# Optimization experiments

Hardware: AMD Instinct MI355X
Metric: run time of the kernel (lower is better)

Reference implementation:

```python
import jax, jax.numpy as jnp
import numpy as np

H = 512          # hidden_size == input_size
K = 32768        # number of child cell inputs (lattice merge fan-in)


def setup_inputs() -> dict:
    key = jax.random.key(0)
    ks = jax.random.split(key, 8)
    s = 1.0 / np.sqrt(H)  # keep matmul outputs O(1)
    return {
        "input_": jax.random.normal(ks[0], (1, H), dtype=jnp.float32),
        "c_input": jax.random.normal(ks[1], (K, H), dtype=jnp.float32),
        "h_0": jax.random.normal(ks[2], (1, H), dtype=jnp.float32),
        "c_0": jax.random.normal(ks[3], (1, H), dtype=jnp.float32),
        "weight_ih": jax.random.normal(ks[4], (H, 3 * H), dtype=jnp.float32) * s,
        "weight_hh": jax.random.normal(ks[5], (H, 3 * H), dtype=jnp.float32) * s,
        "bias": jnp.zeros((3 * H,), dtype=jnp.float32),
        "alpha_weight_ih": jax.random.normal(ks[6], (H, H), dtype=jnp.float32) * s,
        "alpha_weight_hh": jax.random.normal(ks[7], (H, H), dtype=jnp.float32) * s,
    }


def reference(input_, c_input, h_0, c_0, weight_ih, weight_hh, bias,
              alpha_weight_ih, alpha_weight_hh):
    # Gate pre-activations: addmm(bias, h_0, W_hh) + input_ @ W_ih  -> [1, 3H]
    gates = h_0 @ weight_hh + bias + input_ @ weight_ih
    i, o, g = jnp.split(gates, 3, axis=1)        # each [1, H]
    i = jax.nn.sigmoid(i)
    o = jax.nn.sigmoid(o)
    g = jnp.tanh(g)

    # Variable-child softmax-weighted cell merge (non-empty c_input branch)
    alpha_wi = input_ @ alpha_weight_ih          # [1, H], broadcast over K
    alpha_wh = c_input @ alpha_weight_hh         # [K, H]
    alpha = jax.nn.sigmoid(alpha_wi + alpha_wh)  # [K, H]

    logits = jnp.concatenate([i, alpha], axis=0)  # [K+1, H]
    w = jnp.exp(logits)
    w = w / (w.sum(axis=0, keepdims=True) + 1e-12)

    merge = jnp.concatenate([g, c_input], axis=0)  # [K+1, H]
    c_1 = (merge * w).sum(axis=0, keepdims=True)   # [1, H]
    h_1 = o * jnp.tanh(c_1)                        # [1, H]
    return h_1, c_1
```

## Files before the change

### kernel.cpp

```cpp
#include <hip/hip_runtime.h>
#include <hip/hip_bf16.h>
#include <stdint.h>

#define Hdim 512
#define KC   32768

typedef __hip_bfloat16 bf16;
typedef __attribute__((ext_vector_type(8))) short short8;
typedef __attribute__((ext_vector_type(4))) float float4v;

__device__ __forceinline__ unsigned int pack_bf16_trunc(float e0, float e1) {
  union { float f; unsigned int u; } a, b;
  a.f = e0; b.f = e1;
  return __builtin_amdgcn_perm(b.u, a.u, 0x07060302u);
}

__device__ __forceinline__ unsigned long long pack64(float4v v) {
  return (unsigned long long)pack_bf16_trunc(v[0], v[1])
       | ((unsigned long long)pack_bf16_trunc(v[2], v[3]) << 32);
}

__global__ __launch_bounds__(256) void prep_wt_kernel(
    const float* __restrict__ input_, const float* __restrict__ h_0,
    const float* __restrict__ w_ih, const float* __restrict__ w_hh,
    const float* __restrict__ a_w_ih, const float* __restrict__ a_w_hh,
    float* __restrict__ gates, float* __restrict__ awi, bf16* __restrict__ wt) {
  __shared__ float sh[64 * 65];
  const int t = threadIdx.x;
  const int b = blockIdx.x;
  if (b < 32) {
    const int lane = t & 63, wv = t >> 6;
    float* h0s = sh;
    float* ins = sh + 512;
    float* red = sh + 1024;
    for (int i = t; i < 512; i += 256) { h0s[i] = h_0[i]; ins[i] = input_[i]; }
    __syncthreads();
    float acc = 0.f;
    if (b < 24) {
      const int j = b * 64 + lane;
      const float* whh = w_hh + j;
      const float* wih = w_ih + j;
#pragma unroll 16
      for (int i = 0; i < 128; ++i) {
        const int d = wv * 128 + i;
        acc += h0s[d] * whh[(size_t)d * 1536] + ins[d] * wih[(size_t)d * 1536];
      }
    } else {
      const int j = (b - 24) * 64 + lane;
      const float* wai = a_w_ih + j;
#pragma unroll 16
      for (int i = 0; i < 128; ++i) {
        const int d = wv * 128 + i;
        acc += ins[d] * wai[(size_t)d * Hdim];
      }
    }
    red[wv * 64 + lane] = acc;
    __syncthreads();
    if (t < 64) {
      float s = red[t] + red[64 + t] + red[128 + t] + red[192 + t];
      if (b < 24) gates[b * 64 + t] = s;
      else        awi[(b - 24) * 64 + t] = s;
    }
  } else {
    const int bb = b - 32;
    const int d0 = (bb & 7) * 64, h0 = (bb >> 3) * 64;
    const int tx = t & 63, tw = t >> 6;
    float (*tile)[65] = (float (*)[65])sh;
#pragma unroll
    for (int r = 0; r < 16; ++r) {
      const int row = r * 4 + tw;
      tile[row][tx] = a_w_hh[(size_t)(d0 + row) * Hdim + h0 + tx];
    }
    __syncthreads();
#pragma unroll
    for (int r = 0; r < 16; ++r) {
      const int row = r * 4 + tw;
      wt[(size_t)(h0 + row) * Hdim + d0 + tx] = __float2bfloat16(tile[tx][row]);
    }
  }
}

__global__ __launch_bounds__(256, 3) void gemm_reduce_kernel(
    const float* __restrict__ c_input, const bf16* __restrict__ WT,
    const float* __restrict__ awi,
    float* __restrict__ pw, float* __restrict__ pwc) {
  __shared__ __align__(16) bf16 As[128 * 64];
  __shared__ __align__(16) bf16 Bs[128 * 64];
  __shared__ float red_w[2][128];
  __shared__ float red_wc[2][128];

  const int tid  = threadIdx.x;
  const int lane = tid & 63;
  const int wave = tid >> 6;
  const int wm   = wave & 1;
  const int wn   = wave >> 1;
  const int lm   = lane & 15;
  const int lq   = lane >> 4;

  const int id     = blockIdx.x;
  const int kk_idx = ((id >> 5) << 3) | (id & 7);
  const int h_idx  = (id >> 3) & 3;
  const int kk0 = kk_idx * 128;
  const int h0  = h_idx * 128;

  char* AsB = (char*)As;
  char* BsB = (char*)Bs;

  const int sub   = tid & 15;
  const int rbase = tid >> 4;
  const float* aglob = c_input + (size_t)(kk0 + rbase) * Hdim + sub * 4;
  const int a_lds = rbase * 128 + (((sub >> 1) ^ (rbase & 7)) * 16) + (sub & 1) * 8;

  const int brow0 = wave * 8 + (lane >> 3);
  const int bg    = lane & 7;
  const bf16* bglob = WT + (size_t)(h0 + brow0) * Hdim + bg * 8;
  const int b_lds = brow0 * 128 + ((bg ^ (lane >> 3)) * 16);

  float4v acc[4][4];
#pragma unroll
  for (int i = 0; i < 4; ++i)
#pragma unroll
    for (int j = 0; j < 4; ++j)
      acc[i][j] = (float4v){0.f, 0.f, 0.f, 0.f};

  float4v ap[8];
  short8  bp[4];

#pragma unroll
  for (int j = 0; j < 8; ++j)
    ap[j] = *(const float4v*)(aglob + j * 16 * Hdim);
#pragma unroll
  for (int r = 0; r < 4; ++r)
    bp[r] = *(const short8*)(bglob + (size_t)r * 32 * Hdim);
#pragma unroll
  for (int j = 0; j < 8; ++j)
    *(unsigned long long*)(AsB + j * 2048 + a_lds) = pack64(ap[j]);
#pragma unroll
  for (int r = 0; r < 4; ++r)
    *(short8*)(BsB + r * 4096 + b_lds) = bp[r];
  __syncthreads();

  for (int t = 0; t < 8; ++t) {
    const int d0n = (t + 1) * 64;
    if (t < 7) {
#pragma unroll
      for (int j = 0; j < 8; ++j)
        ap[j] = *(const float4v*)(aglob + j * 16 * Hdim + d0n);
#pragma unroll
      for (int r = 0; r < 4; ++r)
        bp[r] = *(const short8*)(bglob + (size_t)r * 32 * Hdim + d0n);
    }
#pragma unroll
    for (int ks = 0; ks < 2; ++ks) {
      short8 a[4], bfr[4];
#pragma unroll
      for (int mt = 0; mt < 4; ++mt) {
        const int row = wm * 64 + mt * 16 + lm;
        a[mt] = *(const short8*)(AsB + row * 128 + (((ks * 4 + lq) ^ (lm & 7)) * 16));
      }
#pragma unroll
      for (int nt = 0; nt < 4; ++nt) {
        const int row = wn * 64 + nt * 16 + lm;
        bfr[nt] = *(const short8*)(BsB + row * 128 + (((ks * 4 + lq) ^ (lm & 7)) * 16));
      }
#pragma unroll
      for (int mt = 0; mt < 4; ++mt)
#pragma unroll
        for (int nt = 0; nt < 4; ++nt)
          acc[mt][nt] = __builtin_amdgcn_mfma_f32_16x16x32_bf16(a[mt], bfr[nt], acc[mt][nt], 0, 0, 0);
    }
    __syncthreads();
    if (t < 7) {
#pragma unroll
      for (int j = 0; j < 8; ++j)
        *(unsigned long long*)(AsB + j * 2048 + a_lds) = pack64(ap[j]);
#pragma unroll
      for (int r = 0; r < 4; ++r)
        *(short8*)(BsB + r * 4096 + b_lds) = bp[r];
    }
    __syncthreads();
  }

  float awi_l[4];
#pragma unroll
  for (int nt = 0; nt < 4; ++nt)
    awi_l[nt] = awi[h0 + wn * 64 + nt * 16 + lm];

  float sw[4] = {0.f, 0.f, 0.f, 0.f}, swc[4] = {0.f, 0.f, 0.f, 0.f};
#pragma unroll
  for (int nt = 0; nt < 4; ++nt) {
    const int h = h0 + wn * 64 + nt * 16 + lm;
#pragma unroll
    for (int mt = 0; mt < 4; ++mt) {
      const int kkb = kk0 + wm * 64 + mt * 16 + lq * 4;
#pragma unroll
      for (int r = 0; r < 4; ++r) {
        float v = acc[mt][nt][r] + awi_l[nt];
        float aval = 1.f / (1.f + __expf(-v));
        float e = __expf(aval);
        float c = c_input[(size_t)(kkb + r) * Hdim + h];
        sw[nt]  += e;
        swc[nt] += e * c;
      }
    }
  }
#pragma unroll
  for (int nt = 0; nt < 4; ++nt) {
    sw[nt]  += __shfl_xor(sw[nt], 16, 64);
    sw[nt]  += __shfl_xor(sw[nt], 32, 64);
    swc[nt] += __shfl_xor(swc[nt], 16, 64);
    swc[nt] += __shfl_xor(swc[nt], 32, 64);
  }
  if (lq == 0) {
#pragma unroll
    for (int nt = 0; nt < 4; ++nt) {
      red_w[wm][wn * 64 + nt * 16 + lm]  = sw[nt];
      red_wc[wm][wn * 64 + nt * 16 + lm] = swc[nt];
    }
  }
  __syncthreads();
  if (tid < 128) {
    pw[(size_t)kk_idx * Hdim + h0 + tid]  = red_w[0][tid] + red_w[1][tid];
    pwc[(size_t)kk_idx * Hdim + h0 + tid] = red_wc[0][tid] + red_wc[1][tid];
  }
}

__global__ __launch_bounds__(256) void finalize_kernel(
    const float* __restrict__ pw, const float* __restrict__ pwc,
    const float* __restrict__ gates, const float* __restrict__ bias,
    float* __restrict__ out) {
  __shared__ float rsw[8][32], rswc[8][32];
  const int t = threadIdx.x;
  const int hl = t & 31, q = t >> 5;
  const int hh = blockIdx.x * 32 + hl;
  float sw = 0.f, swc = 0.f;
#pragma unroll 8
  for (int kb = q * 32; kb < q * 32 + 32; ++kb) {
    sw  += pw[(size_t)kb * Hdim + hh];
    swc += pwc[(size_t)kb * Hdim + hh];
  }
  rsw[q][hl] = sw; rswc[q][hl] = swc;
  __syncthreads();
  if (t < 32) {
    const int h = blockIdx.x * 32 + t;
    sw = 0.f; swc = 0.f;
#pragma unroll
    for (int q2 = 0; q2 < 8; ++q2) { sw += rsw[q2][t]; swc += rswc[q2][t]; }
    float ipre = gates[h] + bias[h];
    float opre = gates[Hdim + h] + bias[Hdim + h];
    float gpre = gates[2 * Hdim + h] + bias[2 * Hdim + h];
    float ei = expf(1.f / (1.f + expf(-ipre)));
    float g  = tanhf(gpre);
    float o  = 1.f / (1.f + expf(-opre));
    float denom = ei + sw + 1e-12f;
    float c1 = (ei * g + swc) / denom;
    float h1 = o * tanhf(c1);
    out[h]        = h1;
    out[Hdim + h] = c1;
  }
}

extern "C" void kernel_launch(void* const* d_in, const int* in_sizes, int n_in,
                              void* d_out, int out_size, void* d_ws, size_t ws_size,
                              hipStream_t stream) {
  const float* input_  = (const float*)d_in[0];
  const float* c_input = (const float*)d_in[1];
  const float* h_0     = (const float*)d_in[2];
  const float* w_ih    = (const float*)d_in[4];
  const float* w_hh    = (const float*)d_in[5];
  const float* bias    = (const float*)d_in[6];
  const float* a_w_ih  = (const float*)d_in[7];
  const float* a_w_hh  = (const float*)d_in[8];

  char* ws = (char*)d_ws;
  float* pw    = (float*)ws;
  float* pwc   = (float*)(ws + 512 * 1024);
  float* gates = (float*)(ws + 1024 * 1024);
  float* awi   = (float*)(ws + 1024 * 1024 + 6144);
  bf16*  WT    = (bf16*)(ws + 1024 * 1024 + 8192);

  hipLaunchKernelGGL(prep_wt_kernel, dim3(96), dim3(256), 0, stream,
                     input_, h_0, w_ih, w_hh, a_w_ih, a_w_hh, gates, awi, WT);
  hipLaunchKernelGGL(gemm_reduce_kernel, dim3(1024), dim3(256), 0, stream,
                     c_input, WT, awi, pw, pwc);
  hipLaunchKernelGGL(finalize_kernel, dim3(16), dim3(256), 0, stream,
                     pw, pwc, gates, bias, (float*)d_out);
}
```

Baseline: 153.3 us.

## Load GEMM fragments directly from global memory into registers, bypassing LDS

```diff
diff --git a/kernel.cpp b/kernel.cpp
--- a/kernel.cpp
+++ b/kernel.cpp
@@ -13,11 +13,6 @@
   union { float f; unsigned int u; } a, b;
   a.f = e0; b.f = e1;
   return __builtin_amdgcn_perm(b.u, a.u, 0x07060302u);
-}
-
-__device__ __forceinline__ unsigned long long pack64(float4v v) {
-  return (unsigned long long)pack_bf16_trunc(v[0], v[1])
-       | ((unsigned long long)pack_bf16_trunc(v[2], v[3]) << 32);
 }
 
 __global__ __launch_bounds__(256) void prep_wt_kernel(
@@ -80,12 +75,10 @@
   }
 }
 
-__global__ __launch_bounds__(256, 3) void gemm_reduce_kernel(
+__global__ __launch_bounds__(256, 2) void gemm_reduce_kernel(
     const float* __restrict__ c_input, const bf16* __restrict__ WT,
     const float* __restrict__ awi,
     float* __restrict__ pw, float* __restrict__ pwc) {
-  __shared__ __align__(16) bf16 As[128 * 64];
-  __shared__ __align__(16) bf16 Bs[128 * 64];
   __shared__ float red_w[2][128];
   __shared__ float red_wc[2][128];
 
@@ -103,18 +96,14 @@
   const int kk0 = kk_idx * 128;
   const int h0  = h_idx * 128;
 
-  char* AsB = (char*)As;
-  char* BsB = (char*)Bs;
-
-  const int sub   = tid & 15;
-  const int rbase = tid >> 4;
-  const float* aglob = c_input + (size_t)(kk0 + rbase) * Hdim + sub * 4;
-  const int a_lds = rbase * 128 + (((sub >> 1) ^ (rbase & 7)) * 16) + (sub & 1) * 8;
-
-  const int brow0 = wave * 8 + (lane >> 3);
-  const int bg    = lane & 7;
-  const bf16* bglob = WT + (size_t)(h0 + brow0) * Hdim + bg * 8;
-  const int b_lds = brow0 * 128 + ((bg ^ (lane >> 3)) * 16);
+  const float* aptr[4];
+  const bf16*  bptr[4];
+#pragma unroll
+  for (int mt = 0; mt < 4; ++mt)
+    aptr[mt] = c_input + (size_t)(kk0 + wm * 64 + mt * 16 + lm) * Hdim + lq * 8;
+#pragma unroll
+  for (int nt = 0; nt < 4; ++nt)
+    bptr[nt] = WT + (size_t)(h0 + wn * 64 + nt * 16 + lm) * Hdim + lq * 8;
 
   float4v acc[4][4];
 #pragma unroll
@@ -123,63 +112,51 @@
     for (int j = 0; j < 4; ++j)
       acc[i][j] = (float4v){0.f, 0.f, 0.f, 0.f};
 
-  float4v ap[8];
-  short8  bp[4];
-
-#pragma unroll
-  for (int j = 0; j < 8; ++j)
-    ap[j] = *(const float4v*)(aglob + j * 16 * Hdim);
-#pragma unroll
-  for (int r = 0; r < 4; ++r)
-    bp[r] = *(const short8*)(bglob + (size_t)r * 32 * Hdim);
-#pragma unroll
-  for (int j = 0; j < 8; ++j)
-    *(unsigned long long*)(AsB + j * 2048 + a_lds) = pack64(ap[j]);
-#pragma unroll
-  for (int r = 0; r < 4; ++r)
-    *(short8*)(BsB + r * 4096 + b_lds) = bp[r];
-  __syncthreads();
-
-  for (int t = 0; t < 8; ++t) {
-    const int d0n = (t + 1) * 64;
-    if (t < 7) {
-#pragma unroll
-      for (int j = 0; j < 8; ++j)
-        ap[j] = *(const float4v*)(aglob + j * 16 * Hdim + d0n);
-#pragma unroll
-      for (int r = 0; r < 4; ++r)
-        bp[r] = *(const short8*)(bglob + (size_t)r * 32 * Hdim + d0n);
-    }
-#pragma unroll
-    for (int ks = 0; ks < 2; ++ks) {
-      short8 a[4], bfr[4];
-#pragma unroll
-      for (int mt = 0; mt < 4; ++mt) {
-        const int row = wm * 64 + mt * 16 + lm;
-        a[mt] = *(const short8*)(AsB + row * 128 + (((ks * 4 + lq) ^ (lm & 7)) * 16));
-      }
-#pragma unroll
-      for (int nt = 0; nt < 4; ++nt) {
-        const int row = wn * 64 + nt * 16 + lm;
-        bfr[nt] = *(const short8*)(BsB + row * 128 + (((ks * 4 + lq) ^ (lm & 7)) * 16));
-      }
-#pragma unroll
-      for (int mt = 0; mt < 4; ++mt)
-#pragma unroll
-        for (int nt = 0; nt < 4; ++nt)
-          acc[mt][nt] = __builtin_amdgcn_mfma_f32_16x16x32_bf16(a[mt], bfr[nt], acc[mt][nt], 0, 0, 0);
-    }
-    __syncthreads();
-    if (t < 7) {
-#pragma unroll
-      for (int j = 0; j < 8; ++j)
-        *(unsigned long long*)(AsB + j * 2048 + a_lds) = pack64(ap[j]);
-#pragma unroll
-      for (int r = 0; r < 4; ++r)
-        *(short8*)(BsB + r * 4096 + b_lds) = bp[r];
-    }
-    __syncthreads();
-  }
+  float4v A0[8], A1[8];
+  short8  B0[4], B1[4];
+
+#define LOAD_STEP(S, AR, BR)                                          \
+  do {                                                                \
+    _Pragma("unroll")                                                 \
+    for (int mt = 0; mt < 4; ++mt) {                                  \
+      AR[mt * 2]     = *(const float4v*)(aptr[mt] + (S) * 32);        \
+      AR[mt * 2 + 1] = *(const float4v*)(aptr[mt] + (S) * 32 + 4);    \
+    }                                                                 \
+    _Pragma("unroll")                                                 \
+    for (int nt = 0; nt < 4; ++nt)                                    \
+      BR[nt] = *(const short8*)(bptr[nt] + (S) * 32);                 \
+  } while (0)
+
+#define COMPUTE_STEP(AR, BR)                                          \
+  do {                                                                \
+    short8 af[4];                                                     \
+    _Pragma("unroll")                                                 \
+    for (int mt = 0; mt < 4; ++mt) {                                  \
+      union { unsigned int w[4]; short8 s8; } u;                      \
+      u.w[0] = pack_bf16_trunc(AR[mt * 2][0], AR[mt * 2][1]);         \
+      u.w[1] = pack_bf16_trunc(AR[mt * 2][2], AR[mt * 2][3]);         \
+      u.w[2] = pack_bf16_trunc(AR[mt * 2 + 1][0], AR[mt * 2 + 1][1]); \
+      u.w[3] = pack_bf16_trunc(AR[mt * 2 + 1][2], AR[mt * 2 + 1][3]); \
+      af[mt] = u.s8;                                                  \
+    }                                                                 \
+    _Pragma("unroll")                                                 \
+    for (int mt = 0; mt < 4; ++mt)                                    \
+      _Pragma("unroll")                                               \
+      for (int nt = 0; nt < 4; ++nt)                                  \
+        acc[mt][nt] = __builtin_amdgcn_mfma_f32_16x16x32_bf16(        \
+            af[mt], BR[nt], acc[mt][nt], 0, 0, 0);                    \
+  } while (0)
+
+  LOAD_STEP(0, A0, B0);
+#pragma unroll
+  for (int s = 0; s < 16; s += 2) {
+    LOAD_STEP(s + 1, A1, B1);
+    COMPUTE_STEP(A0, B0);
+    if (s + 2 < 16) LOAD_STEP(s + 2, A0, B0);
+    COMPUTE_STEP(A1, B1);
+  }
+#undef LOAD_STEP
+#undef COMPUTE_STEP
 
   float awi_l[4];
 #pragma unroll
```

After: 222.4 us. +45.1%, slower.

## Double-buffer LDS tiles in gemm_reduce to drop one barrier per k-step

Applied to the files above, without the earlier changes.

```diff
diff --git a/kernel.cpp b/kernel.cpp
--- a/kernel.cpp
+++ b/kernel.cpp
@@ -80,12 +80,12 @@
   }
 }
 
-__global__ __launch_bounds__(256, 3) void gemm_reduce_kernel(
+__global__ __launch_bounds__(256) void gemm_reduce_kernel(
     const float* __restrict__ c_input, const bf16* __restrict__ WT,
     const float* __restrict__ awi,
     float* __restrict__ pw, float* __restrict__ pwc) {
-  __shared__ __align__(16) bf16 As[128 * 64];
-  __shared__ __align__(16) bf16 Bs[128 * 64];
+  __shared__ __align__(16) bf16 AsBuf[2][128 * 64];
+  __shared__ __align__(16) bf16 BsBuf[2][128 * 64];
   __shared__ float red_w[2][128];
   __shared__ float red_wc[2][128];
 
@@ -103,17 +103,19 @@
   const int kk0 = kk_idx * 128;
   const int h0  = h_idx * 128;
 
-  char* AsB = (char*)As;
-  char* BsB = (char*)Bs;
+  char* const As0 = (char*)AsBuf[0];
+  char* const As1 = (char*)AsBuf[1];
+  char* const Bs0 = (char*)BsBuf[0];
+  char* const Bs1 = (char*)BsBuf[1];
 
   const int sub   = tid & 15;
   const int rbase = tid >> 4;
-  const float* aglob = c_input + (size_t)(kk0 + rbase) * Hdim + sub * 4;
+  const float* aglobS = c_input + (size_t)(kk0 + rbase) * Hdim + sub * 4;
   const int a_lds = rbase * 128 + (((sub >> 1) ^ (rbase & 7)) * 16) + (sub & 1) * 8;
 
   const int brow0 = wave * 8 + (lane >> 3);
   const int bg    = lane & 7;
-  const bf16* bglob = WT + (size_t)(h0 + brow0) * Hdim + bg * 8;
+  const bf16* bglobS = WT + (size_t)(h0 + brow0) * Hdim + bg * 8;
   const int b_lds = brow0 * 128 + ((bg ^ (lane >> 3)) * 16);
 
   float4v acc[4][4];
@@ -123,63 +125,78 @@
     for (int j = 0; j < 4; ++j)
       acc[i][j] = (float4v){0.f, 0.f, 0.f, 0.f};
 
-  float4v ap[8];
-  short8  bp[4];
-
-#pragma unroll
-  for (int j = 0; j < 8; ++j)
-    ap[j] = *(const float4v*)(aglob + j * 16 * Hdim);
-#pragma unroll
-  for (int r = 0; r < 4; ++r)
-    bp[r] = *(const short8*)(bglob + (size_t)r * 32 * Hdim);
-#pragma unroll
-  for (int j = 0; j < 8; ++j)
-    *(unsigned long long*)(AsB + j * 2048 + a_lds) = pack64(ap[j]);
-#pragma unroll
-  for (int r = 0; r < 4; ++r)
-    *(short8*)(BsB + r * 4096 + b_lds) = bp[r];
+  {
+    float4v ap[8]; short8 bp[4];
+#pragma unroll
+    for (int j = 0; j < 8; ++j)
+      ap[j] = *(const float4v*)(aglobS + j * 16 * Hdim);
+#pragma unroll
+    for (int r = 0; r < 4; ++r)
+      bp[r] = *(const short8*)(bglobS + (size_t)r * 32 * Hdim);
+#pragma unroll
+    for (int j = 0; j < 8; ++j)
+      *(unsigned long long*)(As0 + j * 2048 + a_lds) = pack64(ap[j]);
+#pragma unroll
+    for (int r = 0; r < 4; ++r)
+      *(short8*)(Bs0 + r * 4096 + b_lds) = bp[r];
+  }
   __syncthreads();
 
-  for (int t = 0; t < 8; ++t) {
-    const int d0n = (t + 1) * 64;
-    if (t < 7) {
-#pragma unroll
-      for (int j = 0; j < 8; ++j)
-        ap[j] = *(const float4v*)(aglob + j * 16 * Hdim + d0n);
-#pragma unroll
-      for (int r = 0; r < 4; ++r)
-        bp[r] = *(const short8*)(bglob + (size_t)r * 32 * Hdim + d0n);
-    }
-#pragma unroll
-    for (int ks = 0; ks < 2; ++ks) {
-      short8 a[4], bfr[4];
-#pragma unroll
-      for (int mt = 0; mt < 4; ++mt) {
-        const int row = wm * 64 + mt * 16 + lm;
-        a[mt] = *(const short8*)(AsB + row * 128 + (((ks * 4 + lq) ^ (lm & 7)) * 16));
-      }
-#pragma unroll
-      for (int nt = 0; nt < 4; ++nt) {
-        const int row = wn * 64 + nt * 16 + lm;
-        bfr[nt] = *(const short8*)(BsB + row * 128 + (((ks * 4 + lq) ^ (lm & 7)) * 16));
-      }
-#pragma unroll
-      for (int mt = 0; mt < 4; ++mt)
-#pragma unroll
-        for (int nt = 0; nt < 4; ++nt)
-          acc[mt][nt] = __builtin_amdgcn_mfma_f32_16x16x32_bf16(a[mt], bfr[nt], acc[mt][nt], 0, 0, 0);
-    }
-    __syncthreads();
-    if (t < 7) {
-#pragma unroll
-      for (int j = 0; j < 8; ++j)
-        *(unsigned long long*)(AsB + j * 2048 + a_lds) = pack64(ap[j]);
-#pragma unroll
-      for (int r = 0; r < 4; ++r)
-        *(short8*)(BsB + r * 4096 + b_lds) = bp[r];
-    }
-    __syncthreads();
-  }
+#define GITER(T, RAs, RBs, WAs, WBs, NOT_LAST)                              \
+  do {                                                                      \
+    float4v ap[8]; short8 bp[4];                                            \
+    if (NOT_LAST) {                                                         \
+      const int dn = ((T) + 1) * 64;                                        \
+      _Pragma("unroll")                                                     \
+      for (int j = 0; j < 8; ++j)                                           \
+        ap[j] = *(const float4v*)(aglobS + j * 16 * Hdim + dn);             \
+      _Pragma("unroll")                                                     \
+      for (int r = 0; r < 4; ++r)                                           \
+        bp[r] = *(const short8*)(bglobS + (size_t)r * 32 * Hdim + dn);      \
+    }                                                                       \
+    __builtin_amdgcn_sched_barrier(0);   \
+    _Pragma("unroll")                                                       \
+    for (int ks = 0; ks < 2; ++ks) {                                        \
+      short8 a[4], bfr[4];                                                  \
+      _Pragma("unroll")                                                     \
+      for (int mt = 0; mt < 4; ++mt) {                                      \
+        const int row = wm * 64 + mt * 16 + lm;                             \
+        a[mt] = *(const short8*)(RAs + row * 128 +                          \
+                                 (((ks * 4 + lq) ^ (lm & 7)) * 16));        \
+      }                                                                     \
+      _Pragma("unroll")                                                     \
+      for (int nt = 0; nt < 4; ++nt) {                                      \
+        const int row = wn * 64 + nt * 16 + lm;                             \
+        bfr[nt] = *(const short8*)(RBs + row * 128 +                        \
+                                   (((ks * 4 + lq) ^ (lm & 7)) * 16));      \
+      }                                                                     \
+      _Pragma("unroll")                                                     \
+      for (int mt = 0; mt < 4; ++mt)                                        \
+        _Pragma("unroll")                                                   \
+        for (int nt = 0; nt < 4; ++nt)                                      \
+          acc[mt][nt] = __builtin_amdgcn_mfma_f32_16x16x32_bf16(            \
+              a[mt], bfr[nt], acc[mt][nt], 0, 0, 0);                        \
+    }                                                                       \
+    if (NOT_LAST) {                                                         \
+      _Pragma("unroll")                                                     \
+      for (int j = 0; j < 8; ++j)                                           \
+        *(unsigned long long*)(WAs + j * 2048 + a_lds) = pack64(ap[j]);     \
+      _Pragma("unroll")                                                     \
+      for (int r = 0; r < 4; ++r)                                           \
+        *(short8*)(WBs + r * 4096 + b_lds) = bp[r];                         \
+    }                                                                       \
+    __syncthreads();                                                        \
+  } while (0)
+
+  GITER(0, As0, Bs0, As1, Bs1, 1);
+  GITER(1, As1, Bs1, As0, Bs0, 1);
+  GITER(2, As0, Bs0, As1, Bs1, 1);
+  GITER(3, As1, Bs1, As0, Bs0, 1);
+  GITER(4, As0, Bs0, As1, Bs1, 1);
+  GITER(5, As1, Bs1, As0, Bs0, 1);
+  GITER(6, As0, Bs0, As1, Bs1, 1);
+  GITER(7, As1, Bs1, As0, Bs0, 0);
+#undef GITER
 
   float awi_l[4];
 #pragma unroll
```

After: 147.3 us. 3.9% less time.

## Widen GEMM tile to full hidden dim and stream weights via direct LDS loads

Applied to the files above, without the earlier changes.

```diff
diff --git a/kernel.cpp b/kernel.cpp
--- a/kernel.cpp
+++ b/kernel.cpp
@@ -8,6 +8,9 @@
 typedef __hip_bfloat16 bf16;
 typedef __attribute__((ext_vector_type(8))) short short8;
 typedef __attribute__((ext_vector_type(4))) float float4v;
+
+typedef const __attribute__((address_space(1))) void gvoid;
+typedef __attribute__((address_space(3))) void svoid;
 
 __device__ __forceinline__ unsigned int pack_bf16_trunc(float e0, float e1) {
   union { float f; unsigned int u; } a, b;
@@ -18,6 +21,10 @@
 __device__ __forceinline__ unsigned long long pack64(float4v v) {
   return (unsigned long long)pack_bf16_trunc(v[0], v[1])
        | ((unsigned long long)pack_bf16_trunc(v[2], v[3]) << 32);
+}
+
+__device__ __forceinline__ void gload_lds16(const void* g, void* l) {
+  __builtin_amdgcn_global_load_lds((gvoid*)g, (svoid*)l, 16, 0, 0);
 }
 
 __global__ __launch_bounds__(256) void prep_wt_kernel(
@@ -80,14 +87,16 @@
   }
 }
 
-__global__ __launch_bounds__(256, 3) void gemm_reduce_kernel(
+__global__ __launch_bounds__(512, 2) void gemm_reduce_kernel(
     const float* __restrict__ c_input, const bf16* __restrict__ WT,
     const float* __restrict__ awi,
     float* __restrict__ pw, float* __restrict__ pwc) {
-  __shared__ __align__(16) bf16 As[128 * 64];
-  __shared__ __align__(16) bf16 Bs[128 * 64];
-  __shared__ float red_w[2][128];
-  __shared__ float red_wc[2][128];
+  __shared__ __align__(16) char pool[147456];
+  char* const AsB = pool;
+  char* const Bs0 = pool + 16384;
+  char* const Bs1 = pool + 16384 + 65536;
+  float* const red_w  = (float*)pool;
+  float* const red_wc = (float*)(pool + 4096);
 
   const int tid  = threadIdx.x;
   const int lane = tid & 63;
@@ -97,99 +106,93 @@
   const int lm   = lane & 15;
   const int lq   = lane >> 4;
 
-  const int id     = blockIdx.x;
-  const int kk_idx = ((id >> 5) << 3) | (id & 7);
-  const int h_idx  = (id >> 3) & 3;
+  const int kk_idx = blockIdx.x;
   const int kk0 = kk_idx * 128;
-  const int h0  = h_idx * 128;
-
-  char* AsB = (char*)As;
-  char* BsB = (char*)Bs;
 
   const int sub   = tid & 15;
   const int rbase = tid >> 4;
-  const float* aglob = c_input + (size_t)(kk0 + rbase) * Hdim + sub * 4;
+  const float* aglobS = c_input + (size_t)(kk0 + rbase) * Hdim + sub * 4;
   const int a_lds = rbase * 128 + (((sub >> 1) ^ (rbase & 7)) * 16) + (sub & 1) * 8;
 
-  const int brow0 = wave * 8 + (lane >> 3);
-  const int bg    = lane & 7;
-  const bf16* bglob = WT + (size_t)(h0 + brow0) * Hdim + bg * 8;
-  const int b_lds = brow0 * 128 + ((bg ^ (lane >> 3)) * 16);
-
-  float4v acc[4][4];
+  const bf16* bsrcS = WT + (size_t)(64 * wave + (lane >> 3)) * Hdim
+                         + ((lane & 7) ^ (lane >> 3)) * 8;
+  const int b_lds_wave = wave * 8192;
+
+  float4v acc[4][8];
 #pragma unroll
   for (int i = 0; i < 4; ++i)
 #pragma unroll
+    for (int j = 0; j < 8; ++j)
+      acc[i][j] = (float4v){0.f, 0.f, 0.f, 0.f};
+
+#pragma unroll
+  for (int j = 0; j < 8; ++j)
+    gload_lds16(bsrcS + j * 8 * Hdim, Bs0 + b_lds_wave + j * 1024);
+  {
+    float4v ap[4];
+#pragma unroll
     for (int j = 0; j < 4; ++j)
-      acc[i][j] = (float4v){0.f, 0.f, 0.f, 0.f};
-
-  float4v ap[8];
-  short8  bp[4];
-
-#pragma unroll
-  for (int j = 0; j < 8; ++j)
-    ap[j] = *(const float4v*)(aglob + j * 16 * Hdim);
-#pragma unroll
-  for (int r = 0; r < 4; ++r)
-    bp[r] = *(const short8*)(bglob + (size_t)r * 32 * Hdim);
-#pragma unroll
-  for (int j = 0; j < 8; ++j)
-    *(unsigned long long*)(AsB + j * 2048 + a_lds) = pack64(ap[j]);
-#pragma unroll
-  for (int r = 0; r < 4; ++r)
-    *(short8*)(BsB + r * 4096 + b_lds) = bp[r];
+      ap[j] = *(const float4v*)(aglobS + (size_t)j * 32 * Hdim);
+#pragma unroll
+    for (int j = 0; j < 4; ++j)
+      *(unsigned long long*)(AsB + j * 4096 + a_lds) = pack64(ap[j]);
+  }
   __syncthreads();
 
   for (int t = 0; t < 8; ++t) {
-    const int d0n = (t + 1) * 64;
+    char* const BsR = (t & 1) ? Bs1 : Bs0;
+    char* const BsW = (t & 1) ? Bs0 : Bs1;
+    float4v ap[4];
     if (t < 7) {
+      const int dn = (t + 1) * 64;
 #pragma unroll
       for (int j = 0; j < 8; ++j)
-        ap[j] = *(const float4v*)(aglob + j * 16 * Hdim + d0n);
-#pragma unroll
-      for (int r = 0; r < 4; ++r)
-        bp[r] = *(const short8*)(bglob + (size_t)r * 32 * Hdim + d0n);
-    }
+        gload_lds16(bsrcS + j * 8 * Hdim + dn, BsW + b_lds_wave + j * 1024);
+#pragma unroll
+      for (int j = 0; j < 4; ++j)
+        ap[j] = *(const float4v*)(aglobS + (size_t)j * 32 * Hdim + dn);
+    }
+    __builtin_amdgcn_sched_barrier(0);
 #pragma unroll
     for (int ks = 0; ks < 2; ++ks) {
-      short8 a[4], bfr[4];
+      short8 a[4], bfr[8];
 #pragma unroll
       for (int mt = 0; mt < 4; ++mt) {
         const int row = wm * 64 + mt * 16 + lm;
         a[mt] = *(const short8*)(AsB + row * 128 + (((ks * 4 + lq) ^ (lm & 7)) * 16));
       }
 #pragma unroll
-      for (int nt = 0; nt < 4; ++nt) {
-        const int row = wn * 64 + nt * 16 + lm;
-        bfr[nt] = *(const short8*)(BsB + row * 128 + (((ks * 4 + lq) ^ (lm & 7)) * 16));
+      for (int nt = 0; nt < 8; ++nt) {
+        const int row = wn * 128 + nt * 16 + lm;
+        bfr[nt] = *(const short8*)(BsR + row * 128 + (((ks * 4 + lq) ^ (lm & 7)) * 16));
       }
 #pragma unroll
       for (int mt = 0; mt < 4; ++mt)
 #pragma unroll
-        for (int nt = 0; nt < 4; ++nt)
-          acc[mt][nt] = __builtin_amdgcn_mfma_f32_16x16x32_bf16(a[mt], bfr[nt], acc[mt][nt], 0, 0, 0);
+        for (int nt = 0; nt < 8; ++nt)
+          acc[mt][nt] = __builtin_amdgcn_mfma_f32_16x16x32_bf16(
+              a[mt], bfr[nt], acc[mt][nt], 0, 0, 0);
     }
     __syncthreads();
     if (t < 7) {
 #pragma unroll
-      for (int j = 0; j < 8; ++j)
-        *(unsigned long long*)(AsB + j * 2048 + a_lds) = pack64(ap[j]);
-#pragma unroll
-      for (int r = 0; r < 4; ++r)
-        *(short8*)(BsB + r * 4096 + b_lds) = bp[r];
-    }
-    __syncthreads();
-  }
-
-  float awi_l[4];
-#pragma unroll
-  for (int nt = 0; nt < 4; ++nt)
-    awi_l[nt] = awi[h0 + wn * 64 + nt * 16 + lm];
-
-  float sw[4] = {0.f, 0.f, 0.f, 0.f}, swc[4] = {0.f, 0.f, 0.f, 0.f};
-#pragma unroll
-  for (int nt = 0; nt < 4; ++nt) {
-    const int h = h0 + wn * 64 + nt * 16 + lm;
+      for (int j = 0; j < 4; ++j)
+        *(unsigned long long*)(AsB + j * 4096 + a_lds) = pack64(ap[j]);
+    }
+    __syncthreads();
+  }
+
+  float awi_l[8];
+#pragma unroll
+  for (int nt = 0; nt < 8; ++nt)
+    awi_l[nt] = awi[wn * 128 + nt * 16 + lm];
+
+  float sw[8], swc[8];
+#pragma unroll
+  for (int nt = 0; nt < 8; ++nt) { sw[nt] = 0.f; swc[nt] = 0.f; }
+#pragma unroll
+  for (int nt = 0; nt < 8; ++nt) {
+    const int h = wn * 128 + nt * 16 + lm;
 #pragma unroll
     for (int mt = 0; mt < 4; ++mt) {
       const int kkb = kk0 + wm * 64 + mt * 16 + lq * 4;
@@ -205,7 +208,7 @@
     }
   }
 #pragma unroll
-  for (int nt = 0; nt < 4; ++nt) {
+  for (int nt = 0; nt < 8; ++nt) {
     sw[nt]  += __shfl_xor(sw[nt], 16, 64);
     sw[nt]  += __shfl_xor(sw[nt], 32, 64);
     swc[nt] += __shfl_xor(swc[nt], 16, 64);
@@ -213,16 +216,14 @@
   }
   if (lq == 0) {
 #pragma unroll
-    for (int nt = 0; nt < 4; ++nt) {
-      red_w[wm][wn * 64 + nt * 16 + lm]  = sw[nt];
-      red_wc[wm][wn * 64 + nt * 16 + lm] = swc[nt];
+    for (int nt = 0; nt < 8; ++nt) {
+      red_w[wm * 512 + wn * 128 + nt * 16 + lm]  = sw[nt];
+      red_wc[wm * 512 + wn * 128 + nt * 16 + lm] = swc[nt];
     }
   }
   __syncthreads();
-  if (tid < 128) {
-    pw[(size_t)kk_idx * Hdim + h0 + tid]  = red_w[0][tid] + red_w[1][tid];
-    pwc[(size_t)kk_idx * Hdim + h0 + tid] = red_wc[0][tid] + red_wc[1][tid];
-  }
+  pw[(size_t)kk_idx * Hdim + tid]  = red_w[tid] + red_w[512 + tid];
+  pwc[(size_t)kk_idx * Hdim + tid] = red_wc[tid] + red_wc[512 + tid];
 }
 
 __global__ __launch_bounds__(256) void finalize_kernel(
@@ -281,7 +282,7 @@
 
   hipLaunchKernelGGL(prep_wt_kernel, dim3(96), dim3(256), 0, stream,
                      input_, h_0, w_ih, w_hh, a_w_ih, a_w_hh, gates, awi, WT);
-  hipLaunchKernelGGL(gemm_reduce_kernel, dim3(1024), dim3(256), 0, stream,
+  hipLaunchKernelGGL(gemm_reduce_kernel, dim3(256), dim3(512), 0, stream,
                      c_input, WT, awi, pw, pwc);
   hipLaunchKernelGGL(finalize_kernel, dim3(16), dim3(256), 0, stream,
                      pw, pwc, gates, bias, (float*)d_out);
```

Result: slower. 169.7 us (+10.8%).
